# Kernel tuning notes

Measured on AMD Instinct MI355X. Metric: run time of the kernel, lower is better.

The kernel has to match this reference:

```python
import jax, jax.numpy as jnp
import numpy as np

NUM_USERS = 100000
NUM_ITEMS = 50000
N_NODES = NUM_USERS + NUM_ITEMS
EMB = 64
N_EDGES = 2000000
NUM_LAYERS = 3


def setup_inputs() -> dict:
    key = jax.random.key(0)
    ks = jax.random.split(key, 16)
    inp = {
        "edge_index": jax.random.randint(ks[0], (2, N_EDGES), 0, N_NODES, dtype=jnp.int64 if jax.config.jax_enable_x64 else jnp.int32),
        "user_features": jax.random.normal(ks[1], (NUM_USERS, 15), dtype=jnp.float32),
        "user_color_indices": jax.random.randint(ks[2], (NUM_USERS,), 0, 22),
        "user_size_indices": jax.random.randint(ks[3], (NUM_USERS,), 0, 18),
        "item_features": jax.random.normal(ks[4], (NUM_ITEMS, 17), dtype=jnp.float32),
        "user_emb_w": jax.random.normal(ks[5], (NUM_USERS, EMB), dtype=jnp.float32) * 0.01,
        "item_emb_w": jax.random.normal(ks[6], (NUM_ITEMS, EMB), dtype=jnp.float32) * 0.01,
        "user_numeric_W": jax.random.normal(ks[7], (EMB, 12), dtype=jnp.float32) * 0.1,
        "user_numeric_b": jnp.zeros((EMB,), dtype=jnp.float32),
        "user_vector_W": jax.random.normal(ks[8], (EMB, 3), dtype=jnp.float32) * 0.1,
        "user_vector_b": jnp.zeros((EMB,), dtype=jnp.float32),
        "color_emb_w": jax.random.normal(ks[9], (22, EMB), dtype=jnp.float32) * 0.1,
        "size_emb_w": jax.random.normal(ks[10], (18, EMB), dtype=jnp.float32) * 0.1,
        "item_numeric_W": jax.random.normal(ks[11], (EMB, 5), dtype=jnp.float32) * 0.1,
        "item_numeric_b": jnp.zeros((EMB,), dtype=jnp.float32),
        "item_vector_W": jax.random.normal(ks[12], (EMB, 12), dtype=jnp.float32) * 0.1,
        "item_vector_b": jnp.zeros((EMB,), dtype=jnp.float32),
    }
    return inp


def _lightgcn_conv(x, row, col, norm):
    # gather x at source (row), scale by per-edge norm, scatter-add at target (col)
    msg = norm[:, None] * x[row]                      # [E, d]
    return jax.ops.segment_sum(msg, col, num_segments=N_NODES)


def reference(edge_index, user_features, user_color_indices, user_size_indices,
              item_features, user_emb_w, item_emb_w,
              user_numeric_W, user_numeric_b, user_vector_W, user_vector_b,
              color_emb_w, size_emb_w,
              item_numeric_W, item_numeric_b, item_vector_W, item_vector_b):
    # multimodal feature fusion
    user_emb = (user_emb_w
                + user_features[:, :12] @ user_numeric_W.T + user_numeric_b
                + user_features[:, 12:15] @ user_vector_W.T + user_vector_b
                + color_emb_w[user_color_indices]
                + size_emb_w[user_size_indices])
    item_emb = (item_emb_w
                + item_features[:, :5] @ item_numeric_W.T + item_numeric_b
                + item_features[:, 5:] @ item_vector_W.T + item_vector_b)
    x = jnp.concatenate([user_emb, item_emb], axis=0)  # [N, d]

    row, col = edge_index[0], edge_index[1]
    # symmetric-normalization coefficients (degree over targets, as in source)
    deg = jax.ops.segment_sum(jnp.ones_like(col, dtype=x.dtype), col, num_segments=N_NODES)
    deg_inv_sqrt = jnp.where(deg > 0, jax.lax.rsqrt(jnp.maximum(deg, 1.0)), 0.0)
    norm = deg_inv_sqrt[row] * deg_inv_sqrt[col]       # [E]

    acc = x
    total = x
    for _ in range(NUM_LAYERS):
        acc = _lightgcn_conv(acc, row, col, norm)      # dropout in eval mode = identity
        total = total + acc
    final = total / (NUM_LAYERS + 1)

    return final[:NUM_USERS], final[NUM_USERS:]
```

## Files before the change

### kernel.cpp

```cpp
#include <hip/hip_runtime.h>

#define EMB 64
#define NBMAX 512
#define BCAP 8192
#define BSTRIDE 12288
#define CHUNK 4096


__device__ __forceinline__ unsigned short f2bf(float f) {
    union { float f; unsigned u; } c; c.f = f;
    unsigned r = c.u + 0x7fffu + ((c.u >> 16) & 1u);
    return (unsigned short)(r >> 16);
}
__device__ __forceinline__ float bflo(unsigned u) {
    union { unsigned u; float f; } c; c.u = u << 16; return c.f;
}
__device__ __forceinline__ float bfhi(unsigned u) {
    union { unsigned u; float f; } c; c.u = u & 0xffff0000u; return c.f;
}
__device__ __forceinline__ unsigned pack2(float a, float b) {
    return (unsigned)f2bf(a) | ((unsigned)f2bf(b) << 16);
}


__global__ void init_kernel(unsigned* __restrict__ p, int nz,
                            unsigned* __restrict__ dummyA,
                            unsigned* __restrict__ dummyB) {
    int i = blockIdx.x * blockDim.x + threadIdx.x;
    if (i < nz) p[i] = 0u;
    if (blockIdx.x == 0) {
        int t = threadIdx.x;
        if (t < 32) dummyA[t] = 0u;
        else if (t < 64) dummyB[t - 32] = 0u;
    }
}


__global__ void fuse_users_kernel(const float* __restrict__ feat,
                                  const int* __restrict__ cidx,
                                  const int* __restrict__ sidx,
                                  const float* __restrict__ emb_w,
                                  const float* __restrict__ Wn,
                                  const float* __restrict__ bn,
                                  const float* __restrict__ Wv,
                                  const float* __restrict__ bv,
                                  const float* __restrict__ color_w,
                                  const float* __restrict__ size_w,
                                  const float* __restrict__ dis,
                                  unsigned short* __restrict__ totB,
                                  unsigned short* __restrict__ y0,
                                  int U) {
    int t = blockIdx.x * blockDim.x + threadIdx.x;
    int u = t >> 6, d = t & 63;
    if (u >= U) return;
    const float* f = feat + (size_t)u * 15;
    float acc = emb_w[(size_t)u * EMB + d] + bn[d] + bv[d];
#pragma unroll
    for (int k = 0; k < 12; ++k) acc = fmaf(f[k], Wn[d * 12 + k], acc);
#pragma unroll
    for (int k = 0; k < 3; ++k) acc = fmaf(f[12 + k], Wv[d * 3 + k], acc);
    acc += color_w[(size_t)cidx[u] * EMB + d];
    acc += size_w[(size_t)sidx[u] * EMB + d];
    size_t o = (size_t)u * EMB + d;
    totB[o] = f2bf(acc);
    y0[o] = f2bf(acc * dis[u]);
}

__global__ void fuse_items_kernel(const float* __restrict__ feat,
                                  const float* __restrict__ emb_w,
                                  const float* __restrict__ Wn,
                                  const float* __restrict__ bn,
                                  const float* __restrict__ Wv,
                                  const float* __restrict__ bv,
                                  const float* __restrict__ dis,
                                  unsigned short* __restrict__ totB,
                                  unsigned short* __restrict__ y0,
                                  int I, int U) {
    int t = blockIdx.x * blockDim.x + threadIdx.x;
    int i = t >> 6, d = t & 63;
    if (i >= I) return;
    const float* f = feat + (size_t)i * 17;
    float acc = emb_w[(size_t)i * EMB + d] + bn[d] + bv[d];
#pragma unroll
    for (int k = 0; k < 5; ++k) acc = fmaf(f[k], Wn[d * 5 + k], acc);
#pragma unroll
    for (int k = 0; k < 12; ++k) acc = fmaf(f[5 + k], Wv[d * 12 + k], acc);
    int n = U + i;
    size_t o = (size_t)n * EMB + d;
    totB[o] = f2bf(acc);
    y0[o] = f2bf(acc * dis[n]);
}


__global__ __launch_bounds__(512) void partition_kernel(
        const int* __restrict__ row, const int* __restrict__ col,
        unsigned* __restrict__ bcursor, unsigned* __restrict__ bucketbuf,
        int E, int NB) {
    __shared__ unsigned h[NBMAX];
    __shared__ unsigned wbase[NBMAX];
    const int t = threadIdx.x;
    const long chunk = (long)blockIdx.x * CHUNK;

    for (int i = t; i < NB; i += 512) h[i] = 0u;
    __syncthreads();
    for (int it = 0; it < CHUNK / 512; ++it) {
        long e = chunk + (long)it * 512 + t;
        if (e < E) atomicAdd(&h[((unsigned)col[e]) >> 9], 1u);
    }
    __syncthreads();
    for (int i = t; i < NB; i += 512) {
        unsigned c = h[i];
        wbase[i] = c ? atomicAdd(&bcursor[i], c) : 0u;
    }
    __syncthreads();
    for (int i = t; i < NB; i += 512) h[i] = 0u;
    __syncthreads();
    for (int it = 0; it < CHUNK / 512; ++it) {
        long e = chunk + (long)it * 512 + t;
        if (e < E) {
            unsigned c = (unsigned)col[e];
            unsigned b = c >> 9;
            unsigned lpos = atomicAdd(&h[b], 1u);
            unsigned pos = wbase[b] + lpos;
            if (pos < BCAP)
                bucketbuf[(size_t)b * BCAP + pos] = (((unsigned)row[e]) << 9) | (c & 511u);
        }
    }
}


__global__ __launch_bounds__(512) void bucket_csr_kernel(
        const unsigned* __restrict__ bcursor,
        const unsigned* __restrict__ bucketbuf,
        uint4* __restrict__ meta,
        float* __restrict__ dis, unsigned* __restrict__ srcidx,
        unsigned* __restrict__ clsCnt,
        int N, int NB) {
    const int b = blockIdx.x;
    const int t = threadIdx.x;
    __shared__ unsigned hist[512];
    __shared__ unsigned ps[512];
    __shared__ unsigned cls[64];

    const unsigned base = (unsigned)b * BSTRIDE;
    unsigned cntb = bcursor[b];
    if (cntb > BCAP) cntb = BCAP;

    hist[t] = 0u;
    if (t < 64) cls[t] = 0u;
    __syncthreads();
    const unsigned* buf = bucketbuf + (size_t)b * BCAP;
    for (unsigned j = t; j < cntb; j += 512) atomicAdd(&hist[buf[j] & 511u], 1u);
    __syncthreads();

    unsigned h0 = hist[t];
    unsigned c0p = (h0 + 7u) & ~7u;
    ps[t] = c0p;
    __syncthreads();
    for (int off = 1; off < 512; off <<= 1) {
        unsigned y = (t >= off) ? ps[t - off] : 0u;
        __syncthreads();
        ps[t] += y;
        __syncthreads();
    }
    unsigned beg0 = base + ps[t] - c0p;

    int n0 = (b << 9) + t;
    if (n0 < N) {
        float dv = h0 ? rsqrtf((float)h0) : 0.f;
        meta[n0] = make_uint4(beg0, beg0 + c0p, __float_as_uint(dv), 0u);
        dis[n0] = dv;
        atomicAdd(&cls[min(c0p >> 3, 63u)], 1u);
        for (unsigned k = h0; k < c0p; ++k) srcidx[beg0 + k] = ((unsigned)N) << 5;
    }
    __syncthreads();

    if (t < 64 && cls[t]) atomicAdd(&clsCnt[t], cls[t]);
    hist[t] = beg0;
    __syncthreads();
    for (unsigned j = t; j < cntb; j += 512) {
        unsigned p = buf[j];
        unsigned pos = atomicAdd(&hist[p & 511u], 1u);
        srcidx[pos] = (p >> 9) << 5;
    }
}


__global__ void cls_scan_kernel(const unsigned* __restrict__ clsCnt,
                                unsigned* __restrict__ clsBase) {
    __shared__ unsigned sh[64];
    int t = threadIdx.x;
    if (t < 64) sh[t] = clsCnt[t];
    __syncthreads();
    if (t == 0) {
        unsigned run = 0;
        for (int i = 0; i < 64; ++i) { unsigned v = sh[i]; sh[i] = run; run += v; }
    }
    __syncthreads();
    if (t < 64) clsBase[t] = sh[t];
}


__global__ __launch_bounds__(256) void order_fill_kernel(
        const uint4* __restrict__ meta,
        const unsigned* __restrict__ clsBase, unsigned* __restrict__ clsCur,
        unsigned* __restrict__ order, int N) {
    __shared__ unsigned h[64], wb[64];
    int t = threadIdx.x;
    int n = blockIdx.x * 256 + t;
    if (t < 64) h[t] = 0u;
    __syncthreads();
    unsigned c = 0, lpos = 0;
    bool valid = n < N;
    if (valid) {
        uint4 md = meta[n];
        c = min((md.y - md.x) >> 3, 63u);
        lpos = atomicAdd(&h[c], 1u);
    }
    __syncthreads();
    if (t < 64) wb[t] = h[t] ? atomicAdd(&clsCur[t], h[t]) : 0u;
    __syncthreads();
    if (valid) order[clsBase[c] + wb[c] + lpos] = (unsigned)n;
}


__global__ __launch_bounds__(256) void gather_propagate_kernel(
        const unsigned* __restrict__ order, const uint4* __restrict__ meta,
        const unsigned* __restrict__ src,
        const unsigned* __restrict__ srcidx,
        unsigned* __restrict__ ynext,
        unsigned* __restrict__ totB,
        int N, int store) {
    int lane = threadIdx.x & 63;
    int slot = blockIdx.x * 8 + ((threadIdx.x >> 6) << 1) + (lane >> 5);
    bool active = slot < N;
    int n = active ? (int)order[slot] : 0;
    uint4 md = active ? meta[n] : make_uint4(0u, 0u, 0u, 0u);
    unsigned beg = md.x, endp = md.y;
    float dn = __uint_as_float(md.z);
    unsigned q = (unsigned)((lane >> 4) & 1);
    unsigned m2 = (unsigned)(lane & 15) * 2u;
    float s0 = 0.f, s1 = 0.f, s2 = 0.f, s3 = 0.f;
    float t0 = 0.f, t1 = 0.f, t2 = 0.f, t3 = 0.f;
    unsigned j = beg;
    for (; j + 16 <= endp; j += 16) {
        uint4 iv0 = *reinterpret_cast<const uint4*>(&srcidx[j + 4u * q]);
        uint4 iv1 = *reinterpret_cast<const uint4*>(&srcidx[j + 8u + 4u * q]);
        uint2 ua = *reinterpret_cast<const uint2*>(&src[iv0.x + m2]);
        uint2 ub = *reinterpret_cast<const uint2*>(&src[iv0.y + m2]);
        uint2 uc = *reinterpret_cast<const uint2*>(&src[iv0.z + m2]);
        uint2 ud = *reinterpret_cast<const uint2*>(&src[iv0.w + m2]);
        uint2 ue = *reinterpret_cast<const uint2*>(&src[iv1.x + m2]);
        uint2 uf = *reinterpret_cast<const uint2*>(&src[iv1.y + m2]);
        uint2 ug = *reinterpret_cast<const uint2*>(&src[iv1.z + m2]);
        uint2 uh = *reinterpret_cast<const uint2*>(&src[iv1.w + m2]);
        s0 += (bflo(ua.x) + bflo(ub.x)) + (bflo(uc.x) + bflo(ud.x));
        s1 += (bfhi(ua.x) + bfhi(ub.x)) + (bfhi(uc.x) + bfhi(ud.x));
        s2 += (bflo(ua.y) + bflo(ub.y)) + (bflo(uc.y) + bflo(ud.y));
        s3 += (bfhi(ua.y) + bfhi(ub.y)) + (bfhi(uc.y) + bfhi(ud.y));
        t0 += (bflo(ue.x) + bflo(uf.x)) + (bflo(ug.x) + bflo(uh.x));
        t1 += (bfhi(ue.x) + bfhi(uf.x)) + (bfhi(ug.x) + bfhi(uh.x));
        t2 += (bflo(ue.y) + bflo(uf.y)) + (bflo(ug.y) + bflo(uh.y));
        t3 += (bfhi(ue.y) + bfhi(uf.y)) + (bfhi(ug.y) + bfhi(uh.y));
    }
    if (j < endp) {
        uint4 iv = *reinterpret_cast<const uint4*>(&srcidx[j + 4u * q]);
        uint2 ua = *reinterpret_cast<const uint2*>(&src[iv.x + m2]);
        uint2 ub = *reinterpret_cast<const uint2*>(&src[iv.y + m2]);
        uint2 uc = *reinterpret_cast<const uint2*>(&src[iv.z + m2]);
        uint2 ud = *reinterpret_cast<const uint2*>(&src[iv.w + m2]);
        s0 += (bflo(ua.x) + bflo(ub.x)) + (bflo(uc.x) + bflo(ud.x));
        s1 += (bfhi(ua.x) + bfhi(ub.x)) + (bfhi(uc.x) + bfhi(ud.x));
        s2 += (bflo(ua.y) + bflo(ub.y)) + (bflo(uc.y) + bflo(ud.y));
        s3 += (bfhi(ua.y) + bfhi(ub.y)) + (bfhi(uc.y) + bfhi(ud.y));
    }
    s0 += t0; s1 += t1; s2 += t2; s3 += t3;
    s0 += __shfl_xor(s0, 16);
    s1 += __shfl_xor(s1, 16);
    s2 += __shfl_xor(s2, 16);
    s3 += __shfl_xor(s3, 16);
    if (active && (lane & 31) < 16) {
        float a0 = dn * s0, a1 = dn * s1, a2 = dn * s2, a3 = dn * s3;
        size_t o = (size_t)n * 32 + m2;
        uint2 tv = *reinterpret_cast<const uint2*>(&totB[o]);
        uint2 nv;
        nv.x = pack2(bflo(tv.x) + a0, bfhi(tv.x) + a1);
        nv.y = pack2(bflo(tv.y) + a2, bfhi(tv.y) + a3);
        *reinterpret_cast<uint2*>(&totB[o]) = nv;
        if (store) {
            uint2 pk;
            pk.x = pack2(dn * a0, dn * a1);
            pk.y = pack2(dn * a2, dn * a3);
            *reinterpret_cast<uint2*>(&ynext[(size_t)n * 32 + m2]) = pk;
        }
    }
}


__global__ void finalize_kernel(const unsigned* __restrict__ totB,
                                float2* __restrict__ out2, long n32) {
    long t = (long)blockIdx.x * blockDim.x + threadIdx.x;
    if (t < n32) {
        unsigned u = totB[t];
        out2[t] = make_float2(bflo(u) * 0.25f, bfhi(u) * 0.25f);
    }
}


extern "C" void kernel_launch(void* const* d_in, const int* in_sizes, int n_in,
                              void* d_out, int out_size, void* d_ws, size_t ws_size,
                              hipStream_t stream) {
    const int*   edge       = (const int*)d_in[0];
    const float* user_feat  = (const float*)d_in[1];
    const int*   cidx       = (const int*)d_in[2];
    const int*   sidx       = (const int*)d_in[3];
    const float* item_feat  = (const float*)d_in[4];
    const float* user_emb_w = (const float*)d_in[5];
    const float* item_emb_w = (const float*)d_in[6];
    const float* uWn        = (const float*)d_in[7];
    const float* ubn        = (const float*)d_in[8];
    const float* uWv        = (const float*)d_in[9];
    const float* ubv        = (const float*)d_in[10];
    const float* color_w    = (const float*)d_in[11];
    const float* size_w     = (const float*)d_in[12];
    const float* iWn        = (const float*)d_in[13];
    const float* ibn        = (const float*)d_in[14];
    const float* iWv        = (const float*)d_in[15];
    const float* ibv        = (const float*)d_in[16];

    const int E = in_sizes[0] / 2;
    const int U = in_sizes[5] / EMB;
    const int I = in_sizes[6] / EMB;
    const int N = U + I;
    const int NB = (N + 511) >> 9;

    const int* row = edge;
    const int* col = edge + E;

    unsigned short* yA      = (unsigned short*)d_ws;
    unsigned short* yB      = yA + (size_t)(N + 1) * EMB;
    unsigned*       bucketbuf = (unsigned*)yB;
    unsigned short* totB    = yB + (size_t)(N + 1) * EMB;
    unsigned*       srcidx  = (unsigned*)(totB + (size_t)N * EMB);
    uint4*          meta    = (uint4*)(srcidx + (size_t)NB * BSTRIDE);
    float*          dis     = (float*)(meta + N);
    unsigned*       bcursor = (unsigned*)(dis + N);
    unsigned*       clsCnt  = bcursor + NB;
    unsigned*       clsCur  = clsCnt + 64;
    unsigned*       clsBase = clsCur + 64;
    unsigned*       order   = clsBase + 64;

    const int TB = 256;

    init_kernel<<<(NB + 128 + TB - 1) / TB, TB, 0, stream>>>(
        bcursor, NB + 128,
        (unsigned*)(yA + (size_t)N * EMB), (unsigned*)(yB + (size_t)N * EMB));
    const int gP = (E + CHUNK - 1) / CHUNK;
    partition_kernel<<<gP, 512, 0, stream>>>(row, col, bcursor, bucketbuf, E, NB);
    bucket_csr_kernel<<<NB, 512, 0, stream>>>(bcursor, bucketbuf, meta, dis,
                                              srcidx, clsCnt, N, NB);
    cls_scan_kernel<<<1, 64, 0, stream>>>(clsCnt, clsBase);
    order_fill_kernel<<<(N + TB - 1) / TB, TB, 0, stream>>>(meta, clsBase,
                                                            clsCur, order, N);

    {
        int gU = (int)(((long)U * EMB + TB - 1) / TB);
        fuse_users_kernel<<<gU, TB, 0, stream>>>(user_feat, cidx, sidx, user_emb_w,
                                                 uWn, ubn, uWv, ubv, color_w, size_w,
                                                 dis, totB, yA, U);
        int gI = (int)(((long)I * EMB + TB - 1) / TB);
        fuse_items_kernel<<<gI, TB, 0, stream>>>(item_feat, item_emb_w,
                                                 iWn, ibn, iWv, ibv,
                                                 dis, totB, yA, I, U);
    }

    const int gG = (N + 7) / 8;
    gather_propagate_kernel<<<gG, TB, 0, stream>>>(order, meta,
                                                   (const unsigned*)yA, srcidx,
                                                   (unsigned*)yB, (unsigned*)totB,
                                                   N, 1);
    gather_propagate_kernel<<<gG, TB, 0, stream>>>(order, meta,
                                                   (const unsigned*)yB, srcidx,
                                                   (unsigned*)yA, (unsigned*)totB,
                                                   N, 1);
    gather_propagate_kernel<<<gG, TB, 0, stream>>>(order, meta,
                                                   (const unsigned*)yA, srcidx,
                                                   (unsigned*)yB, (unsigned*)totB,
                                                   N, 0);

    const long n32 = (long)N * 32;
    finalize_kernel<<<(int)((n32 + TB - 1) / TB), TB, 0, stream>>>(
        (const unsigned*)totB, (float2*)d_out, n32);

    (void)n_in; (void)out_size; (void)ws_size;
}
```

Baseline: 259.2 us.

## Fuse degree-class ordering into CSR build and finalize into last propagation layer

The global degree-class ordering, which used a separate scan kernel and a fill kernel, is replaced by a per-bucket local class sort written inside bucket_csr_kernel. This removes two launches and a global atomic pass, at the cost of ordering only within each 512-node bucket rather than globally. The finalize kernel is folded into the last gather layer, which writes the fp32 averaged output directly and skips the bf16 round trip of the running total. The partition kernel now reads col and row four at a time with vector loads.

```diff
diff --git a/kernel.cpp b/kernel.cpp
--- a/kernel.cpp
+++ b/kernel.cpp
@@ -103,9 +103,18 @@
 
     for (int i = t; i < NB; i += 512) h[i] = 0u;
     __syncthreads();
-    for (int it = 0; it < CHUNK / 512; ++it) {
-        long e = chunk + (long)it * 512 + t;
-        if (e < E) atomicAdd(&h[((unsigned)col[e]) >> 9], 1u);
+    for (int it = 0; it < CHUNK / 2048; ++it) {
+        long e = chunk + (long)it * 2048 + t * 4;
+        if (e + 3 < E) {
+            uint4 c4 = *reinterpret_cast<const uint4*>(&col[e]);
+            atomicAdd(&h[c4.x >> 9], 1u); atomicAdd(&h[c4.y >> 9], 1u);
+            atomicAdd(&h[c4.z >> 9], 1u); atomicAdd(&h[c4.w >> 9], 1u);
+        } else {
+            for (int k = 0; k < 4; ++k) {
+                long ek = e + k;
+                if (ek < E) atomicAdd(&h[((unsigned)col[ek]) >> 9], 1u);
+            }
+        }
     }
     __syncthreads();
     for (int i = t; i < NB; i += 512) {
@@ -115,15 +124,32 @@
     __syncthreads();
     for (int i = t; i < NB; i += 512) h[i] = 0u;
     __syncthreads();
-    for (int it = 0; it < CHUNK / 512; ++it) {
-        long e = chunk + (long)it * 512 + t;
-        if (e < E) {
-            unsigned c = (unsigned)col[e];
-            unsigned b = c >> 9;
-            unsigned lpos = atomicAdd(&h[b], 1u);
-            unsigned pos = wbase[b] + lpos;
-            if (pos < BCAP)
-                bucketbuf[(size_t)b * BCAP + pos] = (((unsigned)row[e]) << 9) | (c & 511u);
+    for (int it = 0; it < CHUNK / 2048; ++it) {
+        long e = chunk + (long)it * 2048 + t * 4;
+        if (e + 3 < E) {
+            uint4 c4 = *reinterpret_cast<const uint4*>(&col[e]);
+            uint4 r4 = *reinterpret_cast<const uint4*>(&row[e]);
+            unsigned cs[4] = {c4.x, c4.y, c4.z, c4.w};
+            unsigned rs[4] = {r4.x, r4.y, r4.z, r4.w};
+#pragma unroll
+            for (int k = 0; k < 4; ++k) {
+                unsigned b = cs[k] >> 9;
+                unsigned pos = wbase[b] + atomicAdd(&h[b], 1u);
+                if (pos < BCAP)
+                    bucketbuf[(size_t)b * BCAP + pos] = (rs[k] << 9) | (cs[k] & 511u);
+            }
+        } else {
+            for (int k = 0; k < 4; ++k) {
+                long ek = e + k;
+                if (ek < E) {
+                    unsigned c = (unsigned)col[ek];
+                    unsigned b = c >> 9;
+                    unsigned pos = wbase[b] + atomicAdd(&h[b], 1u);
+                    if (pos < BCAP)
+                        bucketbuf[(size_t)b * BCAP + pos] =
+                            (((unsigned)row[ek]) << 9) | (c & 511u);
+                }
+            }
         }
     }
 }
@@ -134,13 +160,14 @@
         const unsigned* __restrict__ bucketbuf,
         uint4* __restrict__ meta,
         float* __restrict__ dis, unsigned* __restrict__ srcidx,
-        unsigned* __restrict__ clsCnt,
+        unsigned* __restrict__ order,
         int N, int NB) {
     const int b = blockIdx.x;
     const int t = threadIdx.x;
     __shared__ unsigned hist[512];
     __shared__ unsigned ps[512];
     __shared__ unsigned cls[64];
+    __shared__ unsigned clsB[64];
 
     const unsigned base = (unsigned)b * BSTRIDE;
     unsigned cntb = bcursor[b];
@@ -166,16 +193,22 @@
     unsigned beg0 = base + ps[t] - c0p;
 
     int n0 = (b << 9) + t;
+    unsigned c = min(c0p >> 3, 63u), lpos = 0;
     if (n0 < N) {
         float dv = h0 ? rsqrtf((float)h0) : 0.f;
         meta[n0] = make_uint4(beg0, beg0 + c0p, __float_as_uint(dv), 0u);
         dis[n0] = dv;
-        atomicAdd(&cls[min(c0p >> 3, 63u)], 1u);
+        lpos = atomicAdd(&cls[c], 1u);
         for (unsigned k = h0; k < c0p; ++k) srcidx[beg0 + k] = ((unsigned)N) << 5;
     }
     __syncthreads();
-
-    if (t < 64 && cls[t]) atomicAdd(&clsCnt[t], cls[t]);
+    if (t == 0) {
+        unsigned run = 0;
+        for (int i = 0; i < 64; ++i) { unsigned v = cls[i]; clsB[i] = run; run += v; }
+    }
+    __syncthreads();
+    if (n0 < N) order[(b << 9) + clsB[c] + lpos] = (unsigned)n0;
+
     hist[t] = beg0;
     __syncthreads();
     for (unsigned j = t; j < cntb; j += 512) {
@@ -183,44 +216,6 @@
         unsigned pos = atomicAdd(&hist[p & 511u], 1u);
         srcidx[pos] = (p >> 9) << 5;
     }
-}
-
-
-__global__ void cls_scan_kernel(const unsigned* __restrict__ clsCnt,
-                                unsigned* __restrict__ clsBase) {
-    __shared__ unsigned sh[64];
-    int t = threadIdx.x;
-    if (t < 64) sh[t] = clsCnt[t];
-    __syncthreads();
-    if (t == 0) {
-        unsigned run = 0;
-        for (int i = 0; i < 64; ++i) { unsigned v = sh[i]; sh[i] = run; run += v; }
-    }
-    __syncthreads();
-    if (t < 64) clsBase[t] = sh[t];
-}
-
-
-__global__ __launch_bounds__(256) void order_fill_kernel(
-        const uint4* __restrict__ meta,
-        const unsigned* __restrict__ clsBase, unsigned* __restrict__ clsCur,
-        unsigned* __restrict__ order, int N) {
-    __shared__ unsigned h[64], wb[64];
-    int t = threadIdx.x;
-    int n = blockIdx.x * 256 + t;
-    if (t < 64) h[t] = 0u;
-    __syncthreads();
-    unsigned c = 0, lpos = 0;
-    bool valid = n < N;
-    if (valid) {
-        uint4 md = meta[n];
-        c = min((md.y - md.x) >> 3, 63u);
-        lpos = atomicAdd(&h[c], 1u);
-    }
-    __syncthreads();
-    if (t < 64) wb[t] = h[t] ? atomicAdd(&clsCur[t], h[t]) : 0u;
-    __syncthreads();
-    if (valid) order[clsBase[c] + wb[c] + lpos] = (unsigned)n;
 }
 
 
@@ -230,7 +225,8 @@
         const unsigned* __restrict__ srcidx,
         unsigned* __restrict__ ynext,
         unsigned* __restrict__ totB,
-        int N, int store) {
+        float4* __restrict__ outF,
+        int N, int mode) {
     int lane = threadIdx.x & 63;
     int slot = blockIdx.x * 8 + ((threadIdx.x >> 6) << 1) + (lane >> 5);
     bool active = slot < N;
@@ -240,6 +236,8 @@
     float dn = __uint_as_float(md.z);
     unsigned q = (unsigned)((lane >> 4) & 1);
     unsigned m2 = (unsigned)(lane & 15) * 2u;
+    size_t o = (size_t)n * 32 + m2;
+    uint2 tv = *reinterpret_cast<const uint2*>(&totB[o]);
     float s0 = 0.f, s1 = 0.f, s2 = 0.f, s3 = 0.f;
     float t0 = 0.f, t1 = 0.f, t2 = 0.f, t3 = 0.f;
     unsigned j = beg;
@@ -281,28 +279,21 @@
     s3 += __shfl_xor(s3, 16);
     if (active && (lane & 31) < 16) {
         float a0 = dn * s0, a1 = dn * s1, a2 = dn * s2, a3 = dn * s3;
-        size_t o = (size_t)n * 32 + m2;
-        uint2 tv = *reinterpret_cast<const uint2*>(&totB[o]);
-        uint2 nv;
-        nv.x = pack2(bflo(tv.x) + a0, bfhi(tv.x) + a1);
-        nv.y = pack2(bflo(tv.y) + a2, bfhi(tv.y) + a3);
-        *reinterpret_cast<uint2*>(&totB[o]) = nv;
-        if (store) {
+        float b0 = bflo(tv.x) + a0, b1 = bfhi(tv.x) + a1;
+        float b2 = bflo(tv.y) + a2, b3 = bfhi(tv.y) + a3;
+        if (mode == 0) {
+            uint2 nv;
+            nv.x = pack2(b0, b1);
+            nv.y = pack2(b2, b3);
+            *reinterpret_cast<uint2*>(&totB[o]) = nv;
             uint2 pk;
             pk.x = pack2(dn * a0, dn * a1);
             pk.y = pack2(dn * a2, dn * a3);
             *reinterpret_cast<uint2*>(&ynext[(size_t)n * 32 + m2]) = pk;
+        } else {
+            outF[(size_t)n * 16 + (m2 >> 1)] =
+                make_float4(b0 * 0.25f, b1 * 0.25f, b2 * 0.25f, b3 * 0.25f);
         }
-    }
-}
-
-
-__global__ void finalize_kernel(const unsigned* __restrict__ totB,
-                                float2* __restrict__ out2, long n32) {
-    long t = (long)blockIdx.x * blockDim.x + threadIdx.x;
-    if (t < n32) {
-        unsigned u = totB[t];
-        out2[t] = make_float2(bflo(u) * 0.25f, bfhi(u) * 0.25f);
     }
 }
 
@@ -345,23 +336,17 @@
     uint4*          meta    = (uint4*)(srcidx + (size_t)NB * BSTRIDE);
     float*          dis     = (float*)(meta + N);
     unsigned*       bcursor = (unsigned*)(dis + N);
-    unsigned*       clsCnt  = bcursor + NB;
-    unsigned*       clsCur  = clsCnt + 64;
-    unsigned*       clsBase = clsCur + 64;
-    unsigned*       order   = clsBase + 64;
+    unsigned*       order   = bcursor + NB;
 
     const int TB = 256;
 
-    init_kernel<<<(NB + 128 + TB - 1) / TB, TB, 0, stream>>>(
-        bcursor, NB + 128,
+    init_kernel<<<(NB + TB - 1) / TB, TB, 0, stream>>>(
+        bcursor, NB,
         (unsigned*)(yA + (size_t)N * EMB), (unsigned*)(yB + (size_t)N * EMB));
     const int gP = (E + CHUNK - 1) / CHUNK;
     partition_kernel<<<gP, 512, 0, stream>>>(row, col, bcursor, bucketbuf, E, NB);
     bucket_csr_kernel<<<NB, 512, 0, stream>>>(bcursor, bucketbuf, meta, dis,
-                                              srcidx, clsCnt, N, NB);
-    cls_scan_kernel<<<1, 64, 0, stream>>>(clsCnt, clsBase);
-    order_fill_kernel<<<(N + TB - 1) / TB, TB, 0, stream>>>(meta, clsBase,
-                                                            clsCur, order, N);
+                                              srcidx, order, N, NB);
 
     {
         int gU = (int)(((long)U * EMB + TB - 1) / TB);
@@ -378,19 +363,15 @@
     gather_propagate_kernel<<<gG, TB, 0, stream>>>(order, meta,
                                                    (const unsigned*)yA, srcidx,
                                                    (unsigned*)yB, (unsigned*)totB,
-                                                   N, 1);
+                                                   (float4*)d_out, N, 0);
     gather_propagate_kernel<<<gG, TB, 0, stream>>>(order, meta,
                                                    (const unsigned*)yB, srcidx,
                                                    (unsigned*)yA, (unsigned*)totB,
-                                                   N, 1);
+                                                   (float4*)d_out, N, 0);
     gather_propagate_kernel<<<gG, TB, 0, stream>>>(order, meta,
                                                    (const unsigned*)yA, srcidx,
                                                    (unsigned*)yB, (unsigned*)totB,
-                                                   N, 0);
-
-    const long n32 = (long)N * 32;
-    finalize_kernel<<<(int)((n32 + TB - 1) / TB), TB, 0, stream>>>(
-        (const unsigned*)totB, (float2*)d_out, n32);
+                                                   (float4*)d_out, N, 1);
 
     (void)n_in; (void)out_size; (void)ws_size;
 }
```

Result: faster. 236.6 us (-8.8%).
